# Optimization experiments

Hardware: AMD Instinct MI355X
Metric: run time of the kernel (lower is better)

Reference implementation:

```python
import jax, jax.numpy as jnp
import numpy as np

N = 65536   # total sentences
B = 8192    # number of bags (ragged scopes)
C = 1024    # class_dim
R = 100     # rel_num


def setup_inputs() -> dict:
    key = jax.random.key(0)
    k1, k2, k3, k4 = jax.random.split(key, 4)
    X = jax.random.normal(k1, (N, C), jnp.float32)            # post-fc1 sentence reps
    Constraints = jax.random.normal(k2, (R, C), jnp.float32)  # post-fc2 constraint reps
    W = jax.random.normal(k3, (R, C), jnp.float32) * 0.02     # classifier weight
    b = jnp.zeros((R,), jnp.float32)                           # classifier bias
    # ragged scopes: random cut points -> contiguous [start, end) per bag
    rng = np.random.default_rng(0)
    cuts = np.sort(rng.choice(np.arange(1, N), B - 1, replace=False))
    starts = np.concatenate([[0], cuts])
    ends = np.concatenate([cuts, [N]])
    X_Scope = jnp.asarray(np.stack([starts, ends], axis=1), jnp.int32)  # [B, 2]
    X_Rel = jax.random.randint(k4, (B,), 0, R, jnp.int32)               # [B]
    return dict(X=X, Constraints=Constraints, W=W, b=b, X_Scope=X_Scope, X_Rel=X_Rel)


def reference(X, Constraints, W, b, X_Scope, X_Rel):
    n, _ = X.shape
    nb = X_Scope.shape[0]
    # map each sentence to its (contiguous) bag via scope starts
    starts = X_Scope[:, 0]
    seg = jnp.searchsorted(starts, jnp.arange(n, dtype=starts.dtype), side='right') - 1  # [N]
    # per-sentence attention logit against its bag's relation constraint
    Con = Constraints[X_Rel]                                   # [B, C]
    scores = jnp.einsum('nc,nc->n', X, Con[seg])               # [N]
    # numerically-stable per-bag softmax
    m = jax.ops.segment_max(scores, seg, num_segments=nb)      # [B]
    e = jnp.exp(scores - m[seg])                               # [N]
    denom = jax.ops.segment_sum(e, seg, num_segments=nb)       # [B]
    w = e / denom[seg]                                         # [N]
    # attention-weighted bag pooling
    bag = jax.ops.segment_sum(w[:, None] * X, seg, num_segments=nb)  # [B, C]
    # classifier (dropout is identity at eval)
    return bag @ W.T + b                                       # [B, R]
```

## Files before the change

### kernel.cpp

```cpp
#include <hip/hip_runtime.h>
#include <math.h>

#define CDIM 1024
#define RDIM 100
#define NBAGS 8192
#define RPAD 112

typedef float floatx4 __attribute__((ext_vector_type(4)));
typedef short bf16x8 __attribute__((ext_vector_type(8)));

__device__ __forceinline__ float dot4(float4 a, float4 b) {
    return a.x * b.x + a.y * b.y + a.z * b.z + a.w * b.w;
}

__device__ __forceinline__ unsigned short f2bf(float f) {
    unsigned int u = __builtin_bit_cast(unsigned int, f);
    u += 0x7FFFu + ((u >> 16) & 1u);
    return (unsigned short)(u >> 16);
}

#define COMPUTE_ROW(A0, A1, A2, A3)                                          \
    {                                                                        \
        float p = dot4(A0, c0) + dot4(A1, c1) + dot4(A2, c2) + dot4(A3, c3); \
        p += __shfl_xor(p, 1);                                               \
        p += __shfl_xor(p, 2);                                               \
        p += __shfl_xor(p, 4);                                               \
        p += __shfl_xor(p, 8);                                               \
        p += __shfl_xor(p, 16);                                              \
        p += __shfl_xor(p, 32);                                              \
        const float newm = fmaxf(m, p);                                      \
        const float corr = __expf(m - newm);             \
        const float wgt  = __expf(p - newm);                                 \
        denom = fmaf(denom, corr, wgt);                                      \
        a0.x = fmaf(a0.x, corr, wgt * A0.x); a0.y = fmaf(a0.y, corr, wgt * A0.y); \
        a0.z = fmaf(a0.z, corr, wgt * A0.z); a0.w = fmaf(a0.w, corr, wgt * A0.w); \
        a1.x = fmaf(a1.x, corr, wgt * A1.x); a1.y = fmaf(a1.y, corr, wgt * A1.y); \
        a1.z = fmaf(a1.z, corr, wgt * A1.z); a1.w = fmaf(a1.w, corr, wgt * A1.w); \
        a2.x = fmaf(a2.x, corr, wgt * A2.x); a2.y = fmaf(a2.y, corr, wgt * A2.y); \
        a2.z = fmaf(a2.z, corr, wgt * A2.z); a2.w = fmaf(a2.w, corr, wgt * A2.w); \
        a3.x = fmaf(a3.x, corr, wgt * A3.x); a3.y = fmaf(a3.y, corr, wgt * A3.y); \
        a3.z = fmaf(a3.z, corr, wgt * A3.z); a3.w = fmaf(a3.w, corr, wgt * A3.w); \
        m = newm;                                                            \
    }

__global__ __launch_bounds__(256) void bag_softmax_kernel(
    const float* __restrict__ X,
    const float* __restrict__ Constraints,
    const int* __restrict__ scope,
    const int* __restrict__ rel,
    const float* __restrict__ W,
    unsigned short* __restrict__ bagbuf,
    unsigned short* __restrict__ PW)
{
    const int lane = threadIdx.x & 63;
    const int w    = threadIdx.x >> 6;

    if (blockIdx.x >= NBAGS) {
        const int rr = blockIdx.x - NBAGS;
        const int t  = threadIdx.x;
        const int kc  = t >> 3;
        const int sub = (t >> 1) & 3;
        const int i0  = (t & 1) * 4;
        ushort4 o = {0, 0, 0, 0};
        if (rr < RDIM) {
            float4 v = *(const float4*)(W + (size_t)rr * CDIM + t * 4);
            o.x = f2bf(v.x); o.y = f2bf(v.y); o.z = f2bf(v.z); o.w = f2bf(v.w);
        }
        const int tt = rr >> 4, rl = rr & 15;
        *(ushort4*)(PW + ((size_t)(kc * 7 + tt) * 64 + sub * 16 + rl) * 8 + i0) = o;
        return;
    }

    __shared__ float4 lds_acc[4][256];
    __shared__ float  lds_m[4];
    __shared__ float  lds_d[4];

    const int bag = blockIdx.x;
    const int s = scope[2 * bag];
    const int e = scope[2 * bag + 1];
    const int r = rel[bag];

    const float4* conp = (const float4*)(Constraints + (size_t)r * CDIM);
    const float4 c0 = conp[lane];
    const float4 c1 = conp[lane + 64];
    const float4 c2 = conp[lane + 128];
    const float4 c3 = conp[lane + 192];

    float4 a0 = {0.f, 0.f, 0.f, 0.f};
    float4 a1 = {0.f, 0.f, 0.f, 0.f};
    float4 a2 = {0.f, 0.f, 0.f, 0.f};
    float4 a3 = {0.f, 0.f, 0.f, 0.f};
    float m = -INFINITY;
    float denom = 0.f;

    int row = s + w;
    if (row < e) {
        const float4* xp = (const float4*)(X + (size_t)row * CDIM);
        float4 A0 = xp[lane];
        float4 A1 = xp[lane + 64];
        float4 A2 = xp[lane + 128];
        float4 A3 = xp[lane + 192];

        for (; row + 4 < e; row += 4) {
            const float4* np = (const float4*)(X + (size_t)(row + 4) * CDIM);
            float4 B0 = np[lane];
            float4 B1 = np[lane + 64];
            float4 B2 = np[lane + 128];
            float4 B3 = np[lane + 192];
            __builtin_amdgcn_sched_barrier(0);

            COMPUTE_ROW(A0, A1, A2, A3)

            A0 = B0; A1 = B1; A2 = B2; A3 = B3;
        }
        COMPUTE_ROW(A0, A1, A2, A3)
    }

    if (lane == 0) { lds_m[w] = m; lds_d[w] = denom; }
    lds_acc[w][lane]       = a0;
    lds_acc[w][lane + 64]  = a1;
    lds_acc[w][lane + 128] = a2;
    lds_acc[w][lane + 192] = a3;
    __syncthreads();

    const int t = threadIdx.x;
    const float m0 = lds_m[0], m1 = lds_m[1], m2 = lds_m[2], m3 = lds_m[3];
    const float ms = fmaxf(fmaxf(m0, m1), fmaxf(m2, m3));
    const float f0 = __expf(m0 - ms);
    const float f1 = __expf(m1 - ms);
    const float f2 = __expf(m2 - ms);
    const float f3 = __expf(m3 - ms);
    const float dn = f0 * lds_d[0] + f1 * lds_d[1] + f2 * lds_d[2] + f3 * lds_d[3];
    const float inv = 1.0f / dn;

    const float4 v0 = lds_acc[0][t];
    const float4 v1 = lds_acc[1][t];
    const float4 v2 = lds_acc[2][t];
    const float4 v3 = lds_acc[3][t];
    const float ox = (f0 * v0.x + f1 * v1.x + f2 * v2.x + f3 * v3.x) * inv;
    const float oy = (f0 * v0.y + f1 * v1.y + f2 * v2.y + f3 * v3.y) * inv;
    const float oz = (f0 * v0.z + f1 * v1.z + f2 * v2.z + f3 * v3.z) * inv;
    const float ow = (f0 * v0.w + f1 * v1.w + f2 * v2.w + f3 * v3.w) * inv;

    ushort4 o;
    o.x = f2bf(ox); o.y = f2bf(oy); o.z = f2bf(oz); o.w = f2bf(ow);
    *(ushort4*)(bagbuf + (size_t)bag * CDIM + t * 4) = o;
}

__global__ __launch_bounds__(512) void bag_gemm_mfma(
    const unsigned short* __restrict__ bagbuf,
    const unsigned short* __restrict__ PW,
    const float* __restrict__ bias,
    float* __restrict__ out)
{
    const int w    = threadIdx.x >> 6;
    const int q    = w >> 1;
    const int h    = w & 1;
    const int lane = threadIdx.x & 63;
    const int T    = blockIdx.x * 2 + h;
    const int bag0 = T * 16;
    const int ln15 = lane & 15;
    const int koff = (lane >> 4) * 8;

    __shared__ floatx4 lds[8][7][64];

    floatx4 acc[7];
    #pragma unroll
    for (int t = 0; t < 7; ++t) acc[t] = (floatx4){0.f, 0.f, 0.f, 0.f};

    const unsigned short* aRow  = bagbuf + (size_t)(bag0 + ln15) * CDIM + koff;
    const unsigned short* bBase = PW + (size_t)q * 56 * 512 + lane * 8;

    #pragma unroll
    for (int i = 0; i < 8; ++i) {
        const int k0 = (q * 8 + i) * 32;
        const bf16x8 a = *(const bf16x8*)(aRow + k0);
        #pragma unroll
        for (int t = 0; t < 7; ++t) {
            const bf16x8 b = *(const bf16x8*)(bBase + (i * 7 + t) * 512);
            acc[t] = __builtin_amdgcn_mfma_f32_16x16x32_bf16(a, b, acc[t], 0, 0, 0);
        }
    }

    #pragma unroll
    for (int t = 0; t < 7; ++t) lds[w][t][lane] = acc[t];
    __syncthreads();

    #pragma unroll
    for (int p = threadIdx.x; p < 896; p += 512) {
        const int h2   = (p >= 448) ? 1 : 0;
        const int pp   = p - h2 * 448;
        const int t    = pp >> 6;
        const int slot = pp & 63;
        const int r    = t * 16 + (slot & 15);
        if (r < RDIM) {
            floatx4 s = lds[0 + h2][t][slot];
            s += lds[2 + h2][t][slot];
            s += lds[4 + h2][t][slot];
            s += lds[6 + h2][t][slot];
            const float bv = bias[r];
            const int bagr = blockIdx.x * 32 + h2 * 16 + (slot >> 4) * 4;
            out[(size_t)(bagr + 0) * RDIM + r] = s[0] + bv;
            out[(size_t)(bagr + 1) * RDIM + r] = s[1] + bv;
            out[(size_t)(bagr + 2) * RDIM + r] = s[2] + bv;
            out[(size_t)(bagr + 3) * RDIM + r] = s[3] + bv;
        }
    }
}

extern "C" void kernel_launch(void* const* d_in, const int* in_sizes, int n_in,
                              void* d_out, int out_size, void* d_ws, size_t ws_size,
                              hipStream_t stream) {
    const float* X    = (const float*)d_in[0];
    const float* Con  = (const float*)d_in[1];
    const float* W    = (const float*)d_in[2];
    const float* bias = (const float*)d_in[3];
    const int* scope  = (const int*)d_in[4];
    const int* rel    = (const int*)d_in[5];
    float* out = (float*)d_out;

    unsigned short* bagbuf = (unsigned short*)d_ws;
    unsigned short* PW     = bagbuf + (size_t)NBAGS * CDIM;

    bag_softmax_kernel<<<NBAGS + RPAD, 256, 0, stream>>>(X, Con, scope, rel, W, bagbuf, PW);
    bag_gemm_mfma<<<NBAGS / 32, 512, 0, stream>>>(bagbuf, PW, bias, out);
}
```

Baseline: 64.20 us.

## Deepen X row prefetch to two rows and split GEMM K across eight waves

The bag softmax loop now keeps two rows of X in flight per wave instead of one, which hides more global-load latency for the streaming read of X. The cost is extra registers and some tail handling for bags with one or two rows per wave. The bag GEMM now gives each block 16 bags and spreads the K dimension across all 8 waves, with an 8-way LDS reduction. This doubles the block count to improve occupancy and parallelism, in exchange for more reduction work per block.

```diff
diff --git a/kernel.cpp b/kernel.cpp
--- a/kernel.cpp
+++ b/kernel.cpp
@@ -18,6 +18,13 @@
     u += 0x7FFFu + ((u >> 16) & 1u);
     return (unsigned short)(u >> 16);
 }
+
+#define LOADROW(D0, D1, D2, D3, ri)                                          \
+    {                                                                        \
+        const float4* p_ = (const float4*)(X + (size_t)(ri) * CDIM);         \
+        D0 = p_[lane];       D1 = p_[lane + 64];                             \
+        D2 = p_[lane + 128]; D3 = p_[lane + 192];                            \
+    }
 
 #define COMPUTE_ROW(A0, A1, A2, A3)                                          \
     {                                                                        \
@@ -95,25 +102,26 @@
 
     int row = s + w;
     if (row < e) {
-        const float4* xp = (const float4*)(X + (size_t)row * CDIM);
-        float4 A0 = xp[lane];
-        float4 A1 = xp[lane + 64];
-        float4 A2 = xp[lane + 128];
-        float4 A3 = xp[lane + 192];
-
-        for (; row + 4 < e; row += 4) {
-            const float4* np = (const float4*)(X + (size_t)(row + 4) * CDIM);
-            float4 B0 = np[lane];
-            float4 B1 = np[lane + 64];
-            float4 B2 = np[lane + 128];
-            float4 B3 = np[lane + 192];
+        float4 A0, A1, A2, A3;
+        float4 B0, B1, B2, B3;
+        float4 C0, C1, C2, C3;
+
+        LOADROW(A0, A1, A2, A3, row)
+        if (row + 4 < e) LOADROW(B0, B1, B2, B3, row + 4)
+
+        for (; row + 8 < e; row += 4) {
+            LOADROW(C0, C1, C2, C3, row + 8)
             __builtin_amdgcn_sched_barrier(0);
-
             COMPUTE_ROW(A0, A1, A2, A3)
-
             A0 = B0; A1 = B1; A2 = B2; A3 = B3;
-        }
-        COMPUTE_ROW(A0, A1, A2, A3)
+            B0 = C0; B1 = C1; B2 = C2; B3 = C3;
+        }
+        if (row + 4 < e) {
+            COMPUTE_ROW(A0, A1, A2, A3)
+            COMPUTE_ROW(B0, B1, B2, B3)
+        } else {
+            COMPUTE_ROW(A0, A1, A2, A3)
+        }
     }
 
     if (lane == 0) { lds_m[w] = m; lds_d[w] = denom; }
@@ -153,12 +161,9 @@
     const float* __restrict__ bias,
     float* __restrict__ out)
 {
-    const int w    = threadIdx.x >> 6;
-    const int q    = w >> 1;
-    const int h    = w & 1;
+    const int q    = threadIdx.x >> 6;
     const int lane = threadIdx.x & 63;
-    const int T    = blockIdx.x * 2 + h;
-    const int bag0 = T * 16;
+    const int bag0 = blockIdx.x * 16;
     const int ln15 = lane & 15;
     const int koff = (lane >> 4) * 8;
 
@@ -169,37 +174,34 @@
     for (int t = 0; t < 7; ++t) acc[t] = (floatx4){0.f, 0.f, 0.f, 0.f};
 
     const unsigned short* aRow  = bagbuf + (size_t)(bag0 + ln15) * CDIM + koff;
-    const unsigned short* bBase = PW + (size_t)q * 56 * 512 + lane * 8;
+    const unsigned short* bBase = PW + lane * 8;
 
     #pragma unroll
-    for (int i = 0; i < 8; ++i) {
-        const int k0 = (q * 8 + i) * 32;
-        const bf16x8 a = *(const bf16x8*)(aRow + k0);
+    for (int i = 0; i < 4; ++i) {
+        const int kc = q * 4 + i;
+        const bf16x8 a = *(const bf16x8*)(aRow + kc * 32);
         #pragma unroll
         for (int t = 0; t < 7; ++t) {
-            const bf16x8 b = *(const bf16x8*)(bBase + (i * 7 + t) * 512);
+            const bf16x8 b = *(const bf16x8*)(bBase + (size_t)(kc * 7 + t) * 512);
             acc[t] = __builtin_amdgcn_mfma_f32_16x16x32_bf16(a, b, acc[t], 0, 0, 0);
         }
     }
 
     #pragma unroll
-    for (int t = 0; t < 7; ++t) lds[w][t][lane] = acc[t];
+    for (int t = 0; t < 7; ++t) lds[q][t][lane] = acc[t];
     __syncthreads();
 
-    #pragma unroll
-    for (int p = threadIdx.x; p < 896; p += 512) {
-        const int h2   = (p >= 448) ? 1 : 0;
-        const int pp   = p - h2 * 448;
-        const int t    = pp >> 6;
-        const int slot = pp & 63;
+    const int p = threadIdx.x;
+    if (p < 448) {
+        const int t    = p >> 6;
+        const int slot = p & 63;
         const int r    = t * 16 + (slot & 15);
         if (r < RDIM) {
-            floatx4 s = lds[0 + h2][t][slot];
-            s += lds[2 + h2][t][slot];
-            s += lds[4 + h2][t][slot];
-            s += lds[6 + h2][t][slot];
+            floatx4 s = lds[0][t][slot];
+            #pragma unroll
+            for (int qq = 1; qq < 8; ++qq) s += lds[qq][t][slot];
             const float bv = bias[r];
-            const int bagr = blockIdx.x * 32 + h2 * 16 + (slot >> 4) * 4;
+            const int bagr = bag0 + (slot >> 4) * 4;
             out[(size_t)(bagr + 0) * RDIM + r] = s[0] + bv;
             out[(size_t)(bagr + 1) * RDIM + r] = s[1] + bv;
             out[(size_t)(bagr + 2) * RDIM + r] = s[2] + bv;
@@ -223,5 +225,5 @@
     unsigned short* PW     = bagbuf + (size_t)NBAGS * CDIM;
 
     bag_softmax_kernel<<<NBAGS + RPAD, 256, 0, stream>>>(X, Con, scope, rel, W, bagbuf, PW);
-    bag_gemm_mfma<<<NBAGS / 32, 512, 0, stream>>>(bagbuf, PW, bias, out);
-}
+    bag_gemm_mfma<<<NBAGS / 16, 512, 0, stream>>>(bagbuf, PW, bias, out);
+}
```

Result: no change. 63.86 us, median of 2 (-0.5%).
